# Kernel optimization log

Hardware: AMD Instinct MI355X
Metric: run time of the kernel (lower is better)

## Reference

```python
import jax, jax.numpy as jnp
import numpy as np

N = 100000   # nodes
E = 600000   # edges
D = 128      # in_dim == out_dim
ED = 6       # edge_dim
LN_EPS = 1e-5


def setup_inputs() -> dict:
    key = jax.random.key(0)
    ks = jax.random.split(key, 12)
    s = 1.0 / np.sqrt(D)
    se = 1.0 / np.sqrt(ED)
    return {
        "x": jax.random.normal(ks[0], (N, D), dtype=jnp.float32),
        "edge_index": jax.random.randint(ks[1], (2, E), 0, N, dtype=jnp.int64),
        "edge_attr": jax.random.normal(ks[2], (E, ED), dtype=jnp.float32),
        "batch": jnp.zeros((N,), dtype=jnp.int64),
        "W_e": jax.random.uniform(ks[3], (ED, D), jnp.float32, -se, se),
        "b_e": jax.random.uniform(ks[4], (D,), jnp.float32, -se, se),
        "eps": jnp.zeros((), dtype=jnp.float32),  # GINE train_eps init 0
        "W1": jax.random.uniform(ks[5], (D, D), jnp.float32, -s, s),
        "b1": jax.random.uniform(ks[6], (D,), jnp.float32, -s, s),
        "W2": jax.random.uniform(ks[7], (D, D), jnp.float32, -s, s),
        "b2": jax.random.uniform(ks[8], (D,), jnp.float32, -s, s),
        "gamma": jnp.ones((D,), dtype=jnp.float32),
        "beta": jnp.zeros((D,), dtype=jnp.float32),
    }


def reference(x, edge_index, edge_attr, batch, W_e, b_e, eps, W1, b1, W2, b2, gamma, beta):
    src, dst = edge_index[0], edge_index[1]
    # edge embedding: Linear(edge_dim -> in_dim)
    edge_emb = edge_attr @ W_e + b_e                      # [E, D]
    # GINEConv message: ReLU(x_j + edge_emb), scatter-add to target nodes
    msg = jax.nn.relu(x[src] + edge_emb)                  # [E, D]
    agg = jax.ops.segment_sum(msg, dst, num_segments=N)   # [N, D]
    h = (1.0 + eps) * x + agg                             # [N, D]
    # GINE nn: Linear -> ReLU -> Linear
    h = jax.nn.relu(h @ W1 + b1) @ W2 + b2                # [N, D]
    # LayerNorm over feature dim
    mu = jnp.mean(h, axis=-1, keepdims=True)
    var = jnp.var(h, axis=-1, keepdims=True)
    h = (h - mu) * jax.lax.rsqrt(var + LN_EPS) * gamma + beta
    # activation=True -> ReLU; dropout identity in eval mode
    return jax.nn.relu(h)
```

## Files before the change

kernel.cpp:

```cpp
#include <hip/hip_runtime.h>
#include <stdint.h>

#define NN 100000
#define EE 600000
#define DD 128

typedef _Float16 half8 __attribute__((ext_vector_type(8)));
typedef _Float16 h2 __attribute__((ext_vector_type(2)));
typedef float f32x4 __attribute__((ext_vector_type(4)));

__device__ __forceinline__ float pack_h2(float a, float b) {
    h2 h; h.x = (_Float16)a; h.y = (_Float16)b;
    return __builtin_bit_cast(float, h);
}

__global__ __launch_bounds__(256)
void prep_weights(const float* __restrict__ W1, const float* __restrict__ W2,
                  _Float16* __restrict__ w1h, _Float16* __restrict__ w2h,
                  int* __restrict__ zero_base)
{
    int t = blockIdx.x * 256 + threadIdx.x;
    if (zero_base && t < 2 * NN) zero_base[t] = 0;
    if (t >= 2 * DD * DD) return;
    int which = t >> 14;
    int idx = t & (DD * DD - 1);
    int k = idx >> 7;
    int d = idx & 127;
    float wv = (which ? W2 : W1)[k * DD + d];
    int kt = k >> 5, kr = k & 31;
    int grp = kr >> 3, j = kr & 7;
    int nt = d >> 4, cc = d & 15;
    int lane = grp * 16 + cc;
    int off = ((kt * 8 + nt) * 64 + lane) * 8 + j;
    (which ? w2h : w1h)[off] = (_Float16)wv;
}

__global__ __launch_bounds__(256)
void hist_kernel(const int* __restrict__ ei, int* __restrict__ counts)
{
    int e = blockIdx.x * 256 + threadIdx.x;
    if (e < EE) atomicAdd(&counts[ei[EE + e]], 1);
}

__global__ __launch_bounds__(256)
void scan_blocks(const int* __restrict__ counts, int* __restrict__ startv,
                 int* __restrict__ bsum)
{
    const int t = threadIdx.x;
    const int idx = blockIdx.x * 1024 + t * 4;
    int4 v = {0, 0, 0, 0};
    if (idx < NN) v = *(const int4*)(counts + idx);
    int s1 = v.x + v.y, s2 = s1 + v.z, s3 = s2 + v.w;
    const int lane = t & 63;
    int q = s3;
#pragma unroll
    for (int off = 1; off < 64; off <<= 1) {
        int u = __shfl_up(q, off, 64);
        if (lane >= off) q += u;
    }
    __shared__ int wsum[4];
    if (lane == 63) wsum[t >> 6] = q;
    __syncthreads();
    const int w = t >> 6;
    int pre = 0;
    if (w > 0) pre += wsum[0];
    if (w > 1) pre += wsum[1];
    if (w > 2) pre += wsum[2];
    const int excl = (q - s3) + pre;
    if (idx < NN) {
        int4 o = {excl, excl + v.x, excl + s1, excl + s2};
        *(int4*)(startv + idx) = o;
    }
    __syncthreads();
    if (t == 0) bsum[blockIdx.x] = wsum[0] + wsum[1] + wsum[2] + wsum[3];
}

__global__ __launch_bounds__(128)
void scan_top(const int* __restrict__ bsum, int* __restrict__ boff)
{
    __shared__ int sm[128];
    const int t = threadIdx.x;
    const int NB = (NN + 1023) / 1024;
    int v = (t < NB) ? bsum[t] : 0;
    sm[t] = v;
    __syncthreads();
#pragma unroll
    for (int off = 1; off < 128; off <<= 1) {
        int u = (t >= off) ? sm[t - off] : 0;
        __syncthreads();
        sm[t] += u;
        __syncthreads();
    }
    boff[t] = sm[t] - v;
}

__global__ __launch_bounds__(256)
void scatter_rec(const int* __restrict__ ei, const float* __restrict__ ea,
                 const int* __restrict__ start, const int* __restrict__ boff,
                 int* __restrict__ cursor, float* __restrict__ rec)
{
    int e = blockIdx.x * 256 + threadIdx.x;
    if (e >= EE) return;
    int dst = ei[EE + e];
    int src = ei[e];
    int pos = start[dst] + boff[dst >> 10] + atomicAdd(&cursor[dst], 1);
    const float2* eap = (const float2*)(ea + e * 6);
    float2 e01 = eap[0];
    float2 e23 = eap[1];
    float2 e45 = eap[2];
    float4 r;
    r.x = __int_as_float(src);
    r.y = pack_h2(e01.x, e01.y);
    r.z = pack_h2(e23.x, e23.y);
    r.w = pack_h2(e45.x, e45.y);
    *(float4*)(rec + (size_t)pos * 4) = r;
}

#define NWAVE 8192
template<bool H0F16>
__global__ __launch_bounds__(256)
void agg_pers(const float* __restrict__ x, const float* __restrict__ rec,
              const float* __restrict__ We, const float* __restrict__ be,
              const int* __restrict__ start, const int* __restrict__ boff,
              const int* __restrict__ counts, const float* __restrict__ epsp,
              float* __restrict__ h0f, _Float16* __restrict__ h0h)
{
    const int w = blockIdx.x * 4 + (threadIdx.x >> 6);
    const int lane = threadIdx.x & 63;
    const int d0 = lane * 2;
    float2 w0 = *(const float2*)(We + 0 * DD + d0);
    float2 w1 = *(const float2*)(We + 1 * DD + d0);
    float2 w2 = *(const float2*)(We + 2 * DD + d0);
    float2 w3 = *(const float2*)(We + 3 * DD + d0);
    float2 w4 = *(const float2*)(We + 4 * DD + d0);
    float2 w5 = *(const float2*)(We + 5 * DD + d0);
    float2 bb = *(const float2*)(be + d0);
    const float sc = 1.0f + epsp[0];
    const int n0 = (int)(((long long)w * NN) >> 13);
    const int n1 = (int)(((long long)(w + 1) * NN) >> 13);

#define EDGE_ACC2(R, XJ, WGT)                                                   \
    do {                                                                        \
        h2 p01 = __builtin_bit_cast(h2, (R).y);                                 \
        h2 p23 = __builtin_bit_cast(h2, (R).z);                                 \
        h2 p45 = __builtin_bit_cast(h2, (R).w);                                 \
        float f0 = (float)p01.x, f1 = (float)p01.y;                             \
        float f2 = (float)p23.x, f3 = (float)p23.y;                             \
        float f4 = (float)p45.x, f5 = (float)p45.y;                             \
        float tx = (XJ).x + bb.x, ty = (XJ).y + bb.y;                           \
        tx = fmaf(f0, w0.x, tx); ty = fmaf(f0, w0.y, ty);                       \
        tx = fmaf(f1, w1.x, tx); ty = fmaf(f1, w1.y, ty);                       \
        tx = fmaf(f2, w2.x, tx); ty = fmaf(f2, w2.y, ty);                       \
        tx = fmaf(f3, w3.x, tx); ty = fmaf(f3, w3.y, ty);                       \
        tx = fmaf(f4, w4.x, tx); ty = fmaf(f4, w4.y, ty);                       \
        tx = fmaf(f5, w5.x, tx); ty = fmaf(f5, w5.y, ty);                       \
        ax = fmaf((WGT), fmaxf(tx, 0.f), ax);                                   \
        ay = fmaf((WGT), fmaxf(ty, 0.f), ay);                                   \
    } while (0)

    for (int n = n0; n < n1; ++n) {
        const int begin = start[n] + boff[n >> 10];
        const int cnt = counts[n];
        const float4* rp = (const float4*)(rec + (size_t)begin * 4);
        float ax = 0.f, ay = 0.f;
        for (int i = 0; i < cnt; i += 4) {
            const int rem = cnt - i;
            const int ia = i;
            const int ib = i + (rem > 1 ? 1 : 0);
            const int ic = i + (rem > 2 ? 2 : 0);
            const int id = i + (rem > 3 ? 3 : 0);
            float4 ra = rp[ia], rb = rp[ib], rc = rp[ic], rd = rp[id];
            int sa = __float_as_int(ra.x), sb = __float_as_int(rb.x),
                sc2 = __float_as_int(rc.x), sd = __float_as_int(rd.x);
            float2 xa = *(const float2*)(x + (size_t)sa * DD + d0);
            float2 xb = *(const float2*)(x + (size_t)sb * DD + d0);
            float2 xc = *(const float2*)(x + (size_t)sc2 * DD + d0);
            float2 xd = *(const float2*)(x + (size_t)sd * DD + d0);
            const float wb2 = rem > 1 ? 1.f : 0.f;
            const float wc2 = rem > 2 ? 1.f : 0.f;
            const float wd2 = rem > 3 ? 1.f : 0.f;
            EDGE_ACC2(ra, xa, 1.f);
            EDGE_ACC2(rb, xb, wb2);
            EDGE_ACC2(rc, xc, wc2);
            EDGE_ACC2(rd, xd, wd2);
        }
        float2 xn = *(const float2*)(x + (size_t)n * DD + d0);
        float hx = sc * xn.x + ax;
        float hy = sc * xn.y + ay;
        if (H0F16) {
            h2 p; p.x = (_Float16)hx; p.y = (_Float16)hy;
            *(h2*)(h0h + (size_t)n * DD + d0) = p;
        } else {
            float2 o; o.x = hx; o.y = hy;
            *(float2*)(h0f + (size_t)n * DD + d0) = o;
        }
    }
#undef EDGE_ACC2
}

__global__ __launch_bounds__(256)
void edge_kernel(const float* __restrict__ x, const int* __restrict__ ei,
                 const float* __restrict__ ea, const float* __restrict__ We,
                 const float* __restrict__ be, float* agg)
{
    int tid = blockIdx.x * 256 + threadIdx.x;
    int d0 = (tid & 31) * 4;
    float4 w0 = *(const float4*)(We + 0 * DD + d0);
    float4 w1 = *(const float4*)(We + 1 * DD + d0);
    float4 w2 = *(const float4*)(We + 2 * DD + d0);
    float4 w3 = *(const float4*)(We + 3 * DD + d0);
    float4 w4 = *(const float4*)(We + 4 * DD + d0);
    float4 w5 = *(const float4*)(We + 5 * DD + d0);
    float4 bb = *(const float4*)(be + d0);
    int estride = (gridDim.x * 256) >> 5;
    for (int e = tid >> 5; e < EE; e += estride) {
        int src = ei[e];
        int dst = ei[EE + e];
        const float2* eap = (const float2*)(ea + e * 6);
        float2 e01 = eap[0];
        float2 e23 = eap[1];
        float2 e45 = eap[2];
        float4 xj = *(const float4*)(x + (size_t)src * DD + d0);
        float mx = xj.x + bb.x + e01.x*w0.x + e01.y*w1.x + e23.x*w2.x + e23.y*w3.x + e45.x*w4.x + e45.y*w5.x;
        float my = xj.y + bb.y + e01.x*w0.y + e01.y*w1.y + e23.x*w2.y + e23.y*w3.y + e45.x*w4.y + e45.y*w5.y;
        float mz = xj.z + bb.z + e01.x*w0.z + e01.y*w1.z + e23.x*w2.z + e23.y*w3.z + e45.x*w4.z + e45.y*w5.z;
        float mw = xj.w + bb.w + e01.x*w0.w + e01.y*w1.w + e23.x*w2.w + e23.y*w3.w + e45.x*w4.w + e45.y*w5.w;
        float* ap = agg + (size_t)dst * DD + d0;
        atomicAdd(ap + 0, fmaxf(mx, 0.f));
        atomicAdd(ap + 1, fmaxf(my, 0.f));
        atomicAdd(ap + 2, fmaxf(mz, 0.f));
        atomicAdd(ap + 3, fmaxf(mw, 0.f));
    }
}

template<int MODE>
__global__ __launch_bounds__(256)
void node2(const void* __restrict__ h0p, const float* __restrict__ xp,
           const _Float16* __restrict__ w1h, const _Float16* __restrict__ w2h,
           const float* __restrict__ b1, const float* __restrict__ b2,
           const float* __restrict__ gamma, const float* __restrict__ beta,
           const float* __restrict__ epsp, float* __restrict__ out)
{
    __shared__ _Float16 h1buf[4][16 * 128];
    const int wv = threadIdx.x >> 6;
    const int l  = threadIdx.x & 63;
    const int lm = l & 15;
    const int lg = l >> 4;
    const int rbase = blockIdx.x * 128 + wv * 32;

    float gam[8], bet[8];
#pragma unroll
    for (int nt = 0; nt < 8; ++nt) {
        gam[nt] = gamma[nt * 16 + lm];
        bet[nt] = beta[nt * 16 + lm];
    }

    for (int t = 0; t < 2; ++t) {
        const int r0 = rbase + t * 16;
        int arow = r0 + lm;
        if (arow >= NN) arow = NN - 1;

        half8 a1[4];
#pragma unroll
        for (int kt = 0; kt < 4; ++kt) {
            const int kb = kt * 32 + lg * 8;
            if constexpr (MODE == 0) {
                a1[kt] = *(const half8*)((const _Float16*)h0p + (size_t)arow * DD + kb);
            } else {
                const float4* hp = (const float4*)((const float*)h0p + (size_t)arow * DD + kb);
                float4 p0 = hp[0], p1 = hp[1];
                float v[8];
                if constexpr (MODE == 2) {
                    const float scale = 1.0f + epsp[0];
                    const float4* xr = (const float4*)(xp + (size_t)arow * DD + kb);
                    float4 x0 = xr[0], x1 = xr[1];
                    v[0]=x0.x*scale+p0.x; v[1]=x0.y*scale+p0.y; v[2]=x0.z*scale+p0.z; v[3]=x0.w*scale+p0.w;
                    v[4]=x1.x*scale+p1.x; v[5]=x1.y*scale+p1.y; v[6]=x1.z*scale+p1.z; v[7]=x1.w*scale+p1.w;
                } else {
                    v[0]=p0.x; v[1]=p0.y; v[2]=p0.z; v[3]=p0.w;
                    v[4]=p1.x; v[5]=p1.y; v[6]=p1.z; v[7]=p1.w;
                }
#pragma unroll
                for (int j = 0; j < 8; ++j) a1[kt][j] = (_Float16)v[j];
            }
        }

        f32x4 acc[8];
#pragma unroll
        for (int nt = 0; nt < 8; ++nt) { acc[nt][0]=0.f; acc[nt][1]=0.f; acc[nt][2]=0.f; acc[nt][3]=0.f; }
#pragma unroll
        for (int kt = 0; kt < 4; ++kt) {
#pragma unroll
            for (int nt = 0; nt < 8; ++nt) {
                half8 bh = *(const half8*)(w1h + ((size_t)((kt * 8 + nt) * 64 + l)) * 8);
                acc[nt] = __builtin_amdgcn_mfma_f32_16x16x32_f16(a1[kt], bh, acc[nt], 0, 0, 0);
            }
        }

        _Float16* hb = h1buf[wv];
#pragma unroll
        for (int nt = 0; nt < 8; ++nt) {
            const int col = nt * 16 + lm;
            const float bias = b1[col];
#pragma unroll
            for (int q = 0; q < 4; ++q) {
                const int row = lg * 4 + q;
                float v1 = fmaxf(acc[nt][q] + bias, 0.f);
                hb[row * 128 + (col ^ ((row & 7) << 4))] = (_Float16)v1;
            }
        }
        __syncthreads();

        half8 a2[4];
        {
            const int sw = (lm & 7) << 4;
            const _Float16* rowp = hb + lm * 128;
#pragma unroll
            for (int kt = 0; kt < 4; ++kt) {
                const int kb = kt * 32 + lg * 8;
                a2[kt] = *(const half8*)(rowp + (kb ^ sw));
            }
        }

        f32x4 acc2[8];
#pragma unroll
        for (int nt = 0; nt < 8; ++nt) { acc2[nt][0]=0.f; acc2[nt][1]=0.f; acc2[nt][2]=0.f; acc2[nt][3]=0.f; }
#pragma unroll
        for (int kt = 0; kt < 4; ++kt) {
#pragma unroll
            for (int nt = 0; nt < 8; ++nt) {
                half8 bh = *(const half8*)(w2h + ((size_t)((kt * 8 + nt) * 64 + l)) * 8);
                acc2[nt] = __builtin_amdgcn_mfma_f32_16x16x32_f16(a2[kt], bh, acc2[nt], 0, 0, 0);
            }
        }

        float vv[8][4];
        float sums[4] = {0,0,0,0}, sqs[4] = {0,0,0,0};
#pragma unroll
        for (int nt = 0; nt < 8; ++nt) {
            const int col = nt * 16 + lm;
            const float bias = b2[col];
#pragma unroll
            for (int q = 0; q < 4; ++q) {
                float v2 = acc2[nt][q] + bias;
                vv[nt][q] = v2;
                sums[q] += v2;
                sqs[q]  += v2 * v2;
            }
        }
#pragma unroll
        for (int m = 1; m < 16; m <<= 1) {
#pragma unroll
            for (int q = 0; q < 4; ++q) {
                sums[q] += __shfl_xor(sums[q], m, 64);
                sqs[q]  += __shfl_xor(sqs[q],  m, 64);
            }
        }
#pragma unroll
        for (int q = 0; q < 4; ++q) {
            const int grow = r0 + lg * 4 + q;
            if (grow < NN) {
                const float mu  = sums[q] * (1.f / 128.f);
                const float var = sqs[q] * (1.f / 128.f) - mu * mu;
                const float rs  = rsqrtf(var + 1e-5f);
#pragma unroll
                for (int nt = 0; nt < 8; ++nt) {
                    out[(size_t)grow * DD + nt * 16 + lm] =
                        fmaxf((vv[nt][q] - mu) * rs * gam[nt] + bet[nt], 0.f);
                }
            }
        }
        __syncthreads();
    }
}

extern "C" void kernel_launch(void* const* d_in, const int* in_sizes, int n_in,
                              void* d_out, int out_size, void* d_ws, size_t ws_size,
                              hipStream_t stream) {
    (void)in_sizes; (void)n_in; (void)out_size;
    const float* x     = (const float*)d_in[0];
    const int*   ei    = (const int*)d_in[1];
    const float* ea    = (const float*)d_in[2];
    const float* We    = (const float*)d_in[4];
    const float* be    = (const float*)d_in[5];
    const float* epsp  = (const float*)d_in[6];
    const float* W1    = (const float*)d_in[7];
    const float* b1    = (const float*)d_in[8];
    const float* W2    = (const float*)d_in[9];
    const float* b2    = (const float*)d_in[10];
    const float* gamma = (const float*)d_in[11];
    const float* beta  = (const float*)d_in[12];
    float* out = (float*)d_out;

    char* ws = (char*)d_ws;
    _Float16* w1h = (_Float16*)ws;
    _Float16* w2h = w1h + DD * DD;
    size_t off = 2 * (size_t)DD * DD * sizeof(_Float16);
    int* counts = (int*)(ws + off);   off += (size_t)NN * 4;
    int* cursor = (int*)(ws + off);   off += (size_t)NN * 4;
    int* start  = (int*)(ws + off);   off += (size_t)NN * 4;
    int* bsum   = (int*)(ws + off);   off += 512;
    int* boff   = (int*)(ws + off);   off += 512;
    float* rec  = (float*)(ws + off); off += (size_t)EE * 16;
    const size_t need1 = off;
    _Float16* h0h = (_Float16*)(ws + off); off += (size_t)NN * DD * sizeof(_Float16);
    const size_t need0 = off;

    const int NBLK = (NN + 1023) / 1024;
    const int node_blocks = (NN + 127) / 128;

    if (ws_size >= need1) {
        const bool f16h0 = (ws_size >= need0);
        prep_weights<<<(2 * NN + 255) / 256, 256, 0, stream>>>(W1, W2, w1h, w2h, counts);
        hist_kernel<<<(EE + 255) / 256, 256, 0, stream>>>(ei, counts);
        scan_blocks<<<NBLK, 256, 0, stream>>>(counts, start, bsum);
        scan_top<<<1, 128, 0, stream>>>(bsum, boff);
        scatter_rec<<<(EE + 255) / 256, 256, 0, stream>>>(ei, ea, start, boff, cursor, rec);
        if (f16h0) {
            agg_pers<true><<<NWAVE / 4, 256, 0, stream>>>(x, rec, We, be, start, boff,
                                                          counts, epsp, nullptr, h0h);
            node2<0><<<node_blocks, 256, 0, stream>>>(h0h, x, w1h, w2h, b1, b2,
                                                      gamma, beta, epsp, out);
        } else {
            agg_pers<false><<<NWAVE / 4, 256, 0, stream>>>(x, rec, We, be, start, boff,
                                                           counts, epsp, out, nullptr);
            node2<1><<<node_blocks, 256, 0, stream>>>(out, x, w1h, w2h, b1, b2,
                                                      gamma, beta, epsp, out);
        }
    } else {
        hipMemsetAsync(d_out, 0, (size_t)NN * DD * sizeof(float), stream);
        prep_weights<<<(2 * DD * DD + 255) / 256, 256, 0, stream>>>(W1, W2, w1h, w2h, nullptr);
        edge_kernel<<<2048, 256, 0, stream>>>(x, ei, ea, We, be, out);
        node2<2><<<node_blocks, 256, 0, stream>>>(out, x, w1h, w2h, b1, b2,
                                                  gamma, beta, epsp, out);
    }
}
```

Baseline: 175.1 us.

## Fuse setup kernels, single-block scan, fp16 gathered x and packed-half edge math

Merges the histogram, weight prep and a new fp32-to-fp16 conversion of x into one setup kernel, and zeroes counters with a memset. The two-level scan becomes a single 1024-thread block scan that also writes start[N], which removes the counts and boff lookups in later kernels. Aggregation gathers x as fp16 and computes the edge embedding with packed half2 FMAs, aiming to halve gather bandwidth and ALU work at some cost in precision. It also drops two __syncthreads from node2, which risks shared-memory races between loop iterations.

```diff
diff --git a/kernel.cpp b/kernel.cpp
--- a/kernel.cpp
+++ b/kernel.cpp
@@ -9,159 +9,140 @@
 typedef _Float16 h2 __attribute__((ext_vector_type(2)));
 typedef float f32x4 __attribute__((ext_vector_type(4)));
 
-__device__ __forceinline__ float pack_h2(float a, float b) {
+static __device__ __forceinline__ uint32_t pack2(float a, float b) {
     h2 h; h.x = (_Float16)a; h.y = (_Float16)b;
-    return __builtin_bit_cast(float, h);
-}
-
-__global__ __launch_bounds__(256)
-void prep_weights(const float* __restrict__ W1, const float* __restrict__ W2,
-                  _Float16* __restrict__ w1h, _Float16* __restrict__ w2h,
-                  int* __restrict__ zero_base)
-{
-    int t = blockIdx.x * 256 + threadIdx.x;
-    if (zero_base && t < 2 * NN) zero_base[t] = 0;
-    if (t >= 2 * DD * DD) return;
-    int which = t >> 14;
-    int idx = t & (DD * DD - 1);
-    int k = idx >> 7;
-    int d = idx & 127;
-    float wv = (which ? W2 : W1)[k * DD + d];
-    int kt = k >> 5, kr = k & 31;
-    int grp = kr >> 3, j = kr & 7;
-    int nt = d >> 4, cc = d & 15;
-    int lane = grp * 16 + cc;
-    int off = ((kt * 8 + nt) * 64 + lane) * 8 + j;
-    (which ? w2h : w1h)[off] = (_Float16)wv;
-}
-
-__global__ __launch_bounds__(256)
-void hist_kernel(const int* __restrict__ ei, int* __restrict__ counts)
-{
-    int e = blockIdx.x * 256 + threadIdx.x;
-    if (e < EE) atomicAdd(&counts[ei[EE + e]], 1);
-}
-
-__global__ __launch_bounds__(256)
-void scan_blocks(const int* __restrict__ counts, int* __restrict__ startv,
-                 int* __restrict__ bsum)
+    return __builtin_bit_cast(uint32_t, h);
+}
+static __device__ __forceinline__ h2 cvt22(float2 f) {
+    h2 r; r.x = (_Float16)f.x; r.y = (_Float16)f.y; return r;
+}
+
+#define NB_HIST ((EE + 255) / 256)
+#define NB_CONV (NN * DD / 4 / 256)
+template<bool CONV>
+__global__ __launch_bounds__(256)
+void setup_kernel(const int* __restrict__ ei, const float* __restrict__ x,
+                  const float* __restrict__ W1, const float* __restrict__ W2,
+                  int* __restrict__ counts, uint32_t* __restrict__ xh,
+                  _Float16* __restrict__ w1h, _Float16* __restrict__ w2h)
+{
+    const int nbc = CONV ? NB_CONV : 0;
+    const int b = blockIdx.x, tid = threadIdx.x;
+    if (b < NB_HIST) {
+        int e = b * 256 + tid;
+        if (e < EE) atomicAdd(&counts[ei[EE + e]], 1);
+    } else if (CONV && b < NB_HIST + nbc) {
+        int i = (b - NB_HIST) * 256 + tid;
+        float4 v = ((const float4*)x)[i];
+        uint2 o; o.x = pack2(v.x, v.y); o.y = pack2(v.z, v.w);
+        ((uint2*)xh)[i] = o;
+    } else {
+        int t = (b - NB_HIST - nbc) * 256 + tid;
+        if (t < 2 * DD * DD) {
+            int which = t >> 14;
+            int idx = t & (DD * DD - 1);
+            int k = idx >> 7, d = idx & 127;
+            float wv = (which ? W2 : W1)[k * DD + d];
+            int kt = k >> 5, kr = k & 31;
+            int grp = kr >> 3, j = kr & 7;
+            int nt = d >> 4, cc = d & 15;
+            int off = ((kt * 8 + nt) * 64 + grp * 16 + cc) * 8 + j;
+            (which ? w2h : w1h)[off] = (_Float16)wv;
+        }
+    }
+}
+
+__global__ __launch_bounds__(1024)
+void scan_full(const int* __restrict__ counts, int* __restrict__ start)
 {
     const int t = threadIdx.x;
-    const int idx = blockIdx.x * 1024 + t * 4;
-    int4 v = {0, 0, 0, 0};
-    if (idx < NN) v = *(const int4*)(counts + idx);
-    int s1 = v.x + v.y, s2 = s1 + v.z, s3 = s2 + v.w;
-    const int lane = t & 63;
-    int q = s3;
+    const int lo = (int)(((long long)t * NN) >> 10);
+    const int hi = (int)(((long long)(t + 1) * NN) >> 10);
+    int s = 0;
+    for (int i = lo; i < hi; ++i) s += counts[i];
+    const int lane = t & 63, w = t >> 6;
+    int q = s;
 #pragma unroll
     for (int off = 1; off < 64; off <<= 1) {
         int u = __shfl_up(q, off, 64);
         if (lane >= off) q += u;
     }
-    __shared__ int wsum[4];
-    if (lane == 63) wsum[t >> 6] = q;
+    __shared__ int wsum[16];
+    if (lane == 63) wsum[w] = q;
     __syncthreads();
-    const int w = t >> 6;
     int pre = 0;
-    if (w > 0) pre += wsum[0];
-    if (w > 1) pre += wsum[1];
-    if (w > 2) pre += wsum[2];
-    const int excl = (q - s3) + pre;
-    if (idx < NN) {
-        int4 o = {excl, excl + v.x, excl + s1, excl + s2};
-        *(int4*)(startv + idx) = o;
-    }
-    __syncthreads();
-    if (t == 0) bsum[blockIdx.x] = wsum[0] + wsum[1] + wsum[2] + wsum[3];
-}
-
-__global__ __launch_bounds__(128)
-void scan_top(const int* __restrict__ bsum, int* __restrict__ boff)
-{
-    __shared__ int sm[128];
-    const int t = threadIdx.x;
-    const int NB = (NN + 1023) / 1024;
-    int v = (t < NB) ? bsum[t] : 0;
-    sm[t] = v;
-    __syncthreads();
-#pragma unroll
-    for (int off = 1; off < 128; off <<= 1) {
-        int u = (t >= off) ? sm[t - off] : 0;
-        __syncthreads();
-        sm[t] += u;
-        __syncthreads();
-    }
-    boff[t] = sm[t] - v;
+    for (int i = 0; i < w; ++i) pre += wsum[i];
+    int excl = pre + q - s;
+    for (int i = lo; i < hi; ++i) { start[i] = excl; excl += counts[i]; }
+    if (t == 1023) start[NN] = excl;
 }
 
 __global__ __launch_bounds__(256)
 void scatter_rec(const int* __restrict__ ei, const float* __restrict__ ea,
-                 const int* __restrict__ start, const int* __restrict__ boff,
-                 int* __restrict__ cursor, float* __restrict__ rec)
+                 const int* __restrict__ start, int* __restrict__ cursor,
+                 float* __restrict__ rec)
 {
     int e = blockIdx.x * 256 + threadIdx.x;
     if (e >= EE) return;
     int dst = ei[EE + e];
     int src = ei[e];
-    int pos = start[dst] + boff[dst >> 10] + atomicAdd(&cursor[dst], 1);
+    int pos = start[dst] + atomicAdd(&cursor[dst], 1);
     const float2* eap = (const float2*)(ea + e * 6);
     float2 e01 = eap[0];
     float2 e23 = eap[1];
     float2 e45 = eap[2];
     float4 r;
     r.x = __int_as_float(src);
-    r.y = pack_h2(e01.x, e01.y);
-    r.z = pack_h2(e23.x, e23.y);
-    r.w = pack_h2(e45.x, e45.y);
+    r.y = __uint_as_float(pack2(e01.x, e01.y));
+    r.z = __uint_as_float(pack2(e23.x, e23.y));
+    r.w = __uint_as_float(pack2(e45.x, e45.y));
     *(float4*)(rec + (size_t)pos * 4) = r;
 }
 
 #define NWAVE 8192
-template<bool H0F16>
-__global__ __launch_bounds__(256)
-void agg_pers(const float* __restrict__ x, const float* __restrict__ rec,
-              const float* __restrict__ We, const float* __restrict__ be,
-              const int* __restrict__ start, const int* __restrict__ boff,
-              const int* __restrict__ counts, const float* __restrict__ epsp,
-              float* __restrict__ h0f, _Float16* __restrict__ h0h)
+template<bool XH>
+__global__ __launch_bounds__(256)
+void agg_pk(const float* __restrict__ x, const uint32_t* __restrict__ xh,
+            const float* __restrict__ rec, const float* __restrict__ We,
+            const float* __restrict__ be, const int* __restrict__ start,
+            const float* __restrict__ epsp, uint32_t* __restrict__ h0h)
 {
     const int w = blockIdx.x * 4 + (threadIdx.x >> 6);
     const int lane = threadIdx.x & 63;
     const int d0 = lane * 2;
-    float2 w0 = *(const float2*)(We + 0 * DD + d0);
-    float2 w1 = *(const float2*)(We + 1 * DD + d0);
-    float2 w2 = *(const float2*)(We + 2 * DD + d0);
-    float2 w3 = *(const float2*)(We + 3 * DD + d0);
-    float2 w4 = *(const float2*)(We + 4 * DD + d0);
-    float2 w5 = *(const float2*)(We + 5 * DD + d0);
-    float2 bb = *(const float2*)(be + d0);
+    const h2 w0h = cvt22(*(const float2*)(We + 0 * DD + d0));
+    const h2 w1h = cvt22(*(const float2*)(We + 1 * DD + d0));
+    const h2 w2h = cvt22(*(const float2*)(We + 2 * DD + d0));
+    const h2 w3h = cvt22(*(const float2*)(We + 3 * DD + d0));
+    const h2 w4h = cvt22(*(const float2*)(We + 4 * DD + d0));
+    const h2 w5h = cvt22(*(const float2*)(We + 5 * DD + d0));
+    const h2 bbh = cvt22(*(const float2*)(be + d0));
+    h2 zero2; zero2.x = (_Float16)0.f; zero2.y = (_Float16)0.f;
     const float sc = 1.0f + epsp[0];
     const int n0 = (int)(((long long)w * NN) >> 13);
     const int n1 = (int)(((long long)(w + 1) * NN) >> 13);
 
-#define EDGE_ACC2(R, XJ, WGT)                                                   \
-    do {                                                                        \
-        h2 p01 = __builtin_bit_cast(h2, (R).y);                                 \
-        h2 p23 = __builtin_bit_cast(h2, (R).z);                                 \
-        h2 p45 = __builtin_bit_cast(h2, (R).w);                                 \
-        float f0 = (float)p01.x, f1 = (float)p01.y;                             \
-        float f2 = (float)p23.x, f3 = (float)p23.y;                             \
-        float f4 = (float)p45.x, f5 = (float)p45.y;                             \
-        float tx = (XJ).x + bb.x, ty = (XJ).y + bb.y;                           \
-        tx = fmaf(f0, w0.x, tx); ty = fmaf(f0, w0.y, ty);                       \
-        tx = fmaf(f1, w1.x, tx); ty = fmaf(f1, w1.y, ty);                       \
-        tx = fmaf(f2, w2.x, tx); ty = fmaf(f2, w2.y, ty);                       \
-        tx = fmaf(f3, w3.x, tx); ty = fmaf(f3, w3.y, ty);                       \
-        tx = fmaf(f4, w4.x, tx); ty = fmaf(f4, w4.y, ty);                       \
-        tx = fmaf(f5, w5.x, tx); ty = fmaf(f5, w5.y, ty);                       \
-        ax = fmaf((WGT), fmaxf(tx, 0.f), ax);                                   \
-        ay = fmaf((WGT), fmaxf(ty, 0.f), ay);                                   \
+#define EDGE_PK(R, XV, WGT) do {                                                \
+        h2 c01 = __builtin_bit_cast(h2, (R).y);                                 \
+        h2 c23 = __builtin_bit_cast(h2, (R).z);                                 \
+        h2 c45 = __builtin_bit_cast(h2, (R).w);                                 \
+        h2 emb = bbh, s;                                                        \
+        s.x = c01.x; s.y = c01.x; emb = s * w0h + emb;                          \
+        s.x = c01.y; s.y = c01.y; emb = s * w1h + emb;                          \
+        s.x = c23.x; s.y = c23.x; emb = s * w2h + emb;                          \
+        s.x = c23.y; s.y = c23.y; emb = s * w3h + emb;                          \
+        s.x = c45.x; s.y = c45.x; emb = s * w4h + emb;                          \
+        s.x = c45.y; s.y = c45.y; emb = s * w5h + emb;                          \
+        h2 m = (XV) + emb;                                                      \
+        m = __builtin_elementwise_max(m, zero2);                                \
+        ax = fmaf((WGT), (float)m.x, ax);                                       \
+        ay = fmaf((WGT), (float)m.y, ay);                                       \
     } while (0)
 
     for (int n = n0; n < n1; ++n) {
-        const int begin = start[n] + boff[n >> 10];
-        const int cnt = counts[n];
-        const float4* rp = (const float4*)(rec + (size_t)begin * 4);
+        const int begin = start[n];
+        const int cnt = start[n + 1] - begin;
+        const float4* rp = (const float4*)rec + begin;
         float ax = 0.f, ay = 0.f;
         for (int i = 0; i < cnt; i += 4) {
             const int rem = cnt - i;
@@ -171,31 +152,48 @@
             const int id = i + (rem > 3 ? 3 : 0);
             float4 ra = rp[ia], rb = rp[ib], rc = rp[ic], rd = rp[id];
             int sa = __float_as_int(ra.x), sb = __float_as_int(rb.x),
-                sc2 = __float_as_int(rc.x), sd = __float_as_int(rd.x);
-            float2 xa = *(const float2*)(x + (size_t)sa * DD + d0);
-            float2 xb = *(const float2*)(x + (size_t)sb * DD + d0);
-            float2 xc = *(const float2*)(x + (size_t)sc2 * DD + d0);
-            float2 xd = *(const float2*)(x + (size_t)sd * DD + d0);
-            const float wb2 = rem > 1 ? 1.f : 0.f;
-            const float wc2 = rem > 2 ? 1.f : 0.f;
-            const float wd2 = rem > 3 ? 1.f : 0.f;
-            EDGE_ACC2(ra, xa, 1.f);
-            EDGE_ACC2(rb, xb, wb2);
-            EDGE_ACC2(rc, xc, wc2);
-            EDGE_ACC2(rd, xd, wd2);
+                sc3 = __float_as_int(rc.x), sd = __float_as_int(rd.x);
+            h2 xa, xb, xc, xd;
+            if constexpr (XH) {
+                xa = __builtin_bit_cast(h2, xh[((uint32_t)sa << 6) + lane]);
+                xb = __builtin_bit_cast(h2, xh[((uint32_t)sb << 6) + lane]);
+                xc = __builtin_bit_cast(h2, xh[((uint32_t)sc3 << 6) + lane]);
+                xd = __builtin_bit_cast(h2, xh[((uint32_t)sd << 6) + lane]);
+            } else {
+                xa = cvt22(*(const float2*)(x + (size_t)sa * DD + d0));
+                xb = cvt22(*(const float2*)(x + (size_t)sb * DD + d0));
+                xc = cvt22(*(const float2*)(x + (size_t)sc3 * DD + d0));
+                xd = cvt22(*(const float2*)(x + (size_t)sd * DD + d0));
+            }
+            const float wb = rem > 1 ? 1.f : 0.f;
+            const float wc = rem > 2 ? 1.f : 0.f;
+            const float wd = rem > 3 ? 1.f : 0.f;
+            EDGE_PK(ra, xa, 1.f);
+            EDGE_PK(rb, xb, wb);
+            EDGE_PK(rc, xc, wc);
+            EDGE_PK(rd, xd, wd);
         }
         float2 xn = *(const float2*)(x + (size_t)n * DD + d0);
-        float hx = sc * xn.x + ax;
-        float hy = sc * xn.y + ay;
-        if (H0F16) {
-            h2 p; p.x = (_Float16)hx; p.y = (_Float16)hy;
-            *(h2*)(h0h + (size_t)n * DD + d0) = p;
-        } else {
-            float2 o; o.x = hx; o.y = hy;
-            *(float2*)(h0f + (size_t)n * DD + d0) = o;
-        }
-    }
-#undef EDGE_ACC2
+        h0h[(size_t)n * 64 + lane] = pack2(sc * xn.x + ax, sc * xn.y + ay);
+    }
+#undef EDGE_PK
+}
+
+__global__ __launch_bounds__(256)
+void prep_w(const float* __restrict__ W1, const float* __restrict__ W2,
+            _Float16* __restrict__ w1h, _Float16* __restrict__ w2h)
+{
+    int t = blockIdx.x * 256 + threadIdx.x;
+    if (t >= 2 * DD * DD) return;
+    int which = t >> 14;
+    int idx = t & (DD * DD - 1);
+    int k = idx >> 7, d = idx & 127;
+    float wv = (which ? W2 : W1)[k * DD + d];
+    int kt = k >> 5, kr = k & 31;
+    int grp = kr >> 3, j = kr & 7;
+    int nt = d >> 4, cc = d & 15;
+    int off = ((kt * 8 + nt) * 64 + grp * 16 + cc) * 8 + j;
+    (which ? w2h : w1h)[off] = (_Float16)wv;
 }
 
 __global__ __launch_bounds__(256)
@@ -269,17 +267,11 @@
             } else {
                 const float4* hp = (const float4*)((const float*)h0p + (size_t)arow * DD + kb);
                 float4 p0 = hp[0], p1 = hp[1];
-                float v[8];
-                if constexpr (MODE == 2) {
-                    const float scale = 1.0f + epsp[0];
-                    const float4* xr = (const float4*)(xp + (size_t)arow * DD + kb);
-                    float4 x0 = xr[0], x1 = xr[1];
-                    v[0]=x0.x*scale+p0.x; v[1]=x0.y*scale+p0.y; v[2]=x0.z*scale+p0.z; v[3]=x0.w*scale+p0.w;
-                    v[4]=x1.x*scale+p1.x; v[5]=x1.y*scale+p1.y; v[6]=x1.z*scale+p1.z; v[7]=x1.w*scale+p1.w;
-                } else {
-                    v[0]=p0.x; v[1]=p0.y; v[2]=p0.z; v[3]=p0.w;
-                    v[4]=p1.x; v[5]=p1.y; v[6]=p1.z; v[7]=p1.w;
-                }
+                const float scale = 1.0f + epsp[0];
+                const float4* xr = (const float4*)(xp + (size_t)arow * DD + kb);
+                float4 x0 = xr[0], x1 = xr[1];
+                float v[8] = { x0.x*scale+p0.x, x0.y*scale+p0.y, x0.z*scale+p0.z, x0.w*scale+p0.w,
+                               x1.x*scale+p1.x, x1.y*scale+p1.y, x1.z*scale+p1.z, x1.w*scale+p1.w };
 #pragma unroll
                 for (int j = 0; j < 8; ++j) a1[kt][j] = (_Float16)v[j];
             }
@@ -309,7 +301,6 @@
                 hb[row * 128 + (col ^ ((row & 7) << 4))] = (_Float16)v1;
             }
         }
-        __syncthreads();
 
         half8 a2[4];
         {
@@ -370,7 +361,6 @@
                 }
             }
         }
-        __syncthreads();
     }
 }
 
@@ -398,38 +388,38 @@
     size_t off = 2 * (size_t)DD * DD * sizeof(_Float16);
     int* counts = (int*)(ws + off);   off += (size_t)NN * 4;
     int* cursor = (int*)(ws + off);   off += (size_t)NN * 4;
-    int* start  = (int*)(ws + off);   off += (size_t)NN * 4;
-    int* bsum   = (int*)(ws + off);   off += 512;
-    int* boff   = (int*)(ws + off);   off += 512;
+    int* start  = (int*)(ws + off);   off += ((size_t)NN + 1) * 4;
+    off = (off + 15) & ~(size_t)15;
     float* rec  = (float*)(ws + off); off += (size_t)EE * 16;
-    const size_t need1 = off;
-    _Float16* h0h = (_Float16*)(ws + off); off += (size_t)NN * DD * sizeof(_Float16);
-    const size_t need0 = off;
-
-    const int NBLK = (NN + 1023) / 1024;
+    uint32_t* h0h = (uint32_t*)(ws + off); off += (size_t)NN * DD * 2;
+    const size_t need_h0 = off;
+    uint32_t* xh  = (uint32_t*)(ws + off); off += (size_t)NN * DD * 2;
+    const size_t need_xh = off;
+
     const int node_blocks = (NN + 127) / 128;
 
-    if (ws_size >= need1) {
-        const bool f16h0 = (ws_size >= need0);
-        prep_weights<<<(2 * NN + 255) / 256, 256, 0, stream>>>(W1, W2, w1h, w2h, counts);
-        hist_kernel<<<(EE + 255) / 256, 256, 0, stream>>>(ei, counts);
-        scan_blocks<<<NBLK, 256, 0, stream>>>(counts, start, bsum);
-        scan_top<<<1, 128, 0, stream>>>(bsum, boff);
-        scatter_rec<<<(EE + 255) / 256, 256, 0, stream>>>(ei, ea, start, boff, cursor, rec);
-        if (f16h0) {
-            agg_pers<true><<<NWAVE / 4, 256, 0, stream>>>(x, rec, We, be, start, boff,
-                                                          counts, epsp, nullptr, h0h);
-            node2<0><<<node_blocks, 256, 0, stream>>>(h0h, x, w1h, w2h, b1, b2,
-                                                      gamma, beta, epsp, out);
+    if (ws_size >= need_h0) {
+        const bool conv = (ws_size >= need_xh);
+        hipMemsetAsync(counts, 0, 2 * (size_t)NN * 4, stream);
+        if (conv) {
+            setup_kernel<true><<<NB_HIST + NB_CONV + 128, 256, 0, stream>>>(
+                ei, x, W1, W2, counts, xh, w1h, w2h);
         } else {
-            agg_pers<false><<<NWAVE / 4, 256, 0, stream>>>(x, rec, We, be, start, boff,
-                                                           counts, epsp, out, nullptr);
-            node2<1><<<node_blocks, 256, 0, stream>>>(out, x, w1h, w2h, b1, b2,
-                                                      gamma, beta, epsp, out);
-        }
+            setup_kernel<false><<<NB_HIST + 128, 256, 0, stream>>>(
+                ei, x, W1, W2, counts, xh, w1h, w2h);
+        }
+        scan_full<<<1, 1024, 0, stream>>>(counts, start);
+        scatter_rec<<<(EE + 255) / 256, 256, 0, stream>>>(ei, ea, start, cursor, rec);
+        if (conv) {
+            agg_pk<true><<<NWAVE / 4, 256, 0, stream>>>(x, xh, rec, We, be, start, epsp, h0h);
+        } else {
+            agg_pk<false><<<NWAVE / 4, 256, 0, stream>>>(x, xh, rec, We, be, start, epsp, h0h);
+        }
+        node2<0><<<node_blocks, 256, 0, stream>>>(h0h, x, w1h, w2h, b1, b2,
+                                                  gamma, beta, epsp, out);
     } else {
         hipMemsetAsync(d_out, 0, (size_t)NN * DD * sizeof(float), stream);
-        prep_weights<<<(2 * DD * DD + 255) / 256, 256, 0, stream>>>(W1, W2, w1h, w2h, nullptr);
+        prep_w<<<(2 * DD * DD + 255) / 256, 256, 0, stream>>>(W1, W2, w1h, w2h);
         edge_kernel<<<2048, 256, 0, stream>>>(x, ei, ea, We, be, out);
         node2<2><<<node_blocks, 256, 0, stream>>>(out, x, w1h, w2h, b1, b2,
                                                   gamma, beta, epsp, out);
```

After: 318.7 us. 1.82x slower.
